# Kernel optimization log

Measured on AMD Instinct MI355X. Metric: run time of the kernel, lower is better.

## Reference

```python
import jax, jax.numpy as jnp
import numpy as np

DEGREE = 3
FEATURES = 512
N_BSPLINES = 64
BATCH = 2048
WINDOW = DEGREE + 2  # unfold window size: degree + 2
N_KNOTS = N_BSPLINES + DEGREE + 1


def setup_inputs() -> dict:
    key = jax.random.key(0)
    kx, kw = jax.random.split(key)
    x = jax.random.uniform(kx, (BATCH, FEATURES), dtype=jnp.float32)  # in [0,1] = interval
    # reset_parameter(): linspace over interval broadcast to all features
    knots = jnp.broadcast_to(
        jnp.linspace(0.0, 1.0, N_KNOTS, dtype=jnp.float32), (FEATURES, N_KNOTS)
    )
    # weights are zero-init in the module; use small random values for a meaningful baseline
    weights = jax.random.normal(kw, (FEATURES, N_BSPLINES), dtype=jnp.float32) * 0.1
    return {"x": x, "knots": knots, "weights": weights}


def reference(x, knots, weights):
    # knots.unfold(-1, degree+2, 1) -> (F, N, W) sliding windows
    idx = jnp.arange(N_BSPLINES)[:, None] + jnp.arange(WINDOW)[None, :]  # (N, W)
    kwin = knots[:, idx]  # (F, N, W)
    # relu^degree of (x - knot) differences: (B, F, N, W)
    relu = jnp.maximum(x[..., None, None] - kwin, 0.0) ** DEGREE
    # pairwise knot differences + eye: dif[i, j] = kwin[j] - kwin[i] + delta_ij
    knot_dif = kwin[..., None, :] - kwin[..., :, None] + jnp.eye(WINDOW, dtype=knots.dtype)  # (F, N, W, W)
    coef = 1.0 / jnp.prod(knot_dif, axis=-1)  # (F, N, W) divided-difference coefficients
    spline = jnp.sum(relu * coef, axis=-1)  # vecdot over window -> (B, F, N)
    return jnp.sum(spline * weights, axis=-1)  # vecdot over splines -> (B, F)
```

## Files before the change

### kernel.cpp

```cpp
#include <hip/hip_runtime.h>

#pragma clang fp contract(off)

#define FEATURES   512
#define N_BSPLINES 64
#define N_KNOTS    68
#define WINDOW     5
#define BATCH      2048

#define TF 16
#define TB 64
#define QPT 4
#define NT 256
#define TSTRIDE 516

__device__ __forceinline__ float cube_f32(float r) {
    float s = r * r;
    return s * r;
}

__global__ __launch_bounds__(NT) void bspline_fused(
    const float* __restrict__ x, const float* __restrict__ knots,
    const float* __restrict__ weights, float* __restrict__ out)
{
    __shared__ float kL[N_KNOTS * TF];
    __shared__ float tab[TF * TSTRIDE];

    const int tid  = threadIdx.x;
    const int fblk = blockIdx.x & (FEATURES / TF - 1);
    const int bblk = blockIdx.x >> 5;
    const int f0   = fblk * TF;
    const int b0   = bblk * TB;

    const int ft = tid & (TF - 1);
    const int bt = tid >> 4;

    float xq[QPT];
    #pragma unroll
    for (int q = 0; q < QPT; ++q)
        xq[q] = x[(b0 + bt + q * 16) * FEATURES + f0 + ft];

    for (int e = tid; e < N_KNOTS * TF; e += NT) {
        int ff = e & (TF - 1), t = e >> 4;
        kL[t * TF + ff] = knots[(f0 + ff) * N_KNOTS + t];
    }
    __syncthreads();

    for (int e = tid; e < N_BSPLINES * WINDOW * TF; e += NT) {
        int ff = e & (TF - 1);
        int m  = e >> 4;
        int i = m / WINDOW, j = m % WINDOW;
        float kj = kL[(i + j) * TF + ff];
        float prod = 1.0f;
        #pragma unroll
        for (int b = 0; b < WINDOW; ++b) {
            float df = (b == j) ? 1.0f : (kL[(i + b) * TF + ff] - kj);
            prod = prod * df;
        }
        tab[ff * TSTRIDE + i * 8 + j] = 1.0f / prod;
    }
    for (int e = tid; e < N_BSPLINES * TF; e += NT) {
        int ff = e & (TF - 1);
        int i  = e >> 4;
        tab[ff * TSTRIDE + i * 8 + 5] = weights[(f0 + ff) * N_BSPLINES + i];
        tab[ff * TSTRIDE + i * 8 + 6] =
            (i < N_BSPLINES - 1) ? kL[(i + 5) * TF + ff] : 0.0f;
    }
    __syncthreads();

    const float* __restrict__ row = &tab[ft * TSTRIDE];

    float acc[QPT], r0[QPT], r1[QPT], r2[QPT], r3[QPT], r4[QPT];
    #pragma unroll
    for (int q = 0; q < QPT; ++q) {
        acc[q] = 0.0f;
        r0[q] = cube_f32(fmaxf(xq[q] - kL[0 * TF + ft], 0.0f));
        r1[q] = cube_f32(fmaxf(xq[q] - kL[1 * TF + ft], 0.0f));
        r2[q] = cube_f32(fmaxf(xq[q] - kL[2 * TF + ft], 0.0f));
        r3[q] = cube_f32(fmaxf(xq[q] - kL[3 * TF + ft], 0.0f));
        r4[q] = cube_f32(fmaxf(xq[q] - kL[4 * TF + ft], 0.0f));
    }

    #pragma unroll 8
    for (int i = 0; i < N_BSPLINES; ++i) {
        const float4 cv = *(const float4*)&row[i * 8];
        const float4 cw = *(const float4*)&row[i * 8 + 4];
        #pragma unroll
        for (int q = 0; q < QPT; ++q) {
            float m0 = r0[q] * cv.x;
            float m1 = r1[q] * cv.y;
            float m2 = r2[q] * cv.z;
            float m3 = r3[q] * cv.w;
            float m4 = r4[q] * cw.x;
            float t04  = m0 + m4;
            float t042 = t04 + m2;
            float t13  = m1 + m3;
            float sp   = t042 + t13;
            acc[q] = acc[q] + sp * cw.y;
            r0[q] = r1[q]; r1[q] = r2[q]; r2[q] = r3[q]; r3[q] = r4[q];
            r4[q] = cube_f32(fmaxf(xq[q] - cw.z, 0.0f));
        }
    }

    #pragma unroll
    for (int q = 0; q < QPT; ++q)
        out[(b0 + bt + q * 16) * FEATURES + f0 + ft] = acc[q];
}

extern "C" void kernel_launch(void* const* d_in, const int* in_sizes, int n_in,
                              void* d_out, int out_size, void* d_ws, size_t ws_size,
                              hipStream_t stream) {
    const float* x       = (const float*)d_in[0];
    const float* knots   = (const float*)d_in[1];
    const float* weights = (const float*)d_in[2];
    float*       out     = (float*)d_out;

    const int blocks = (FEATURES / TF) * (BATCH / TB);
    bspline_fused<<<blocks, NT, 0, stream>>>(x, knots, weights, out);
}
```

Measured before the change: 89.91 us.

## Split coefficient table into prep kernel and double per-thread batch work

Moves the divided-difference coefficient, weight and knot table construction into a separate per-feature prep kernel that writes to workspace. The eval kernel then copies the ready table into shared memory with float4 loads instead of recomputing it in every batch block. Batch rows per block and per thread are doubled to amortize the table load. The register rotation is unrolled manually so the shifts between window registers disappear. This adds a second kernel launch and roughly doubles live registers per thread, which may lower occupancy.

```diff
diff --git a/kernel.cpp b/kernel.cpp
--- a/kernel.cpp
+++ b/kernel.cpp
@@ -9,8 +9,8 @@
 #define BATCH      2048
 
 #define TF 16
-#define TB 64
-#define QPT 4
+#define TB 128
+#define QPT 8
 #define NT 256
 #define TSTRIDE 516
 
@@ -19,11 +19,53 @@
     return s * r;
 }
 
-__global__ __launch_bounds__(NT) void bspline_fused(
+__global__ __launch_bounds__(320) void bspline_prep(
+    const float* __restrict__ knots, const float* __restrict__ weights,
+    float* __restrict__ g)
+{
+    const int f = blockIdx.x;
+    const int t = threadIdx.x;
+    const float* kf = knots + f * N_KNOTS;
+    const int i = t / WINDOW, j = t % WINDOW;
+    float kj = kf[i + j];
+    float prod = 1.0f;
+    #pragma unroll
+    for (int b = 0; b < WINDOW; ++b) {
+        float df = (b == j) ? 1.0f : (kf[i + b] - kj);
+        prod = prod * df;
+    }
+    g[f * TSTRIDE + i * 8 + j] = 1.0f / prod;
+    if (t < N_BSPLINES) {
+        g[f * TSTRIDE + t * 8 + 5] = weights[f * N_BSPLINES + t];
+        g[f * TSTRIDE + t * 8 + 6] = (t < N_BSPLINES - 1) ? kf[t + 5] : 0.0f;
+        g[f * TSTRIDE + t * 8 + 7] = 0.0f;
+    }
+}
+
+#define STEP(I, RA, RB, RC, RD, RE)                                         \
+    do {                                                                    \
+        const float4 cv = *(const float4*)&row[(I) * 8];        \
+        const float4 cw = *(const float4*)&row[(I) * 8 + 4];   \
+        _Pragma("unroll")                                                   \
+        for (int q = 0; q < QPT; ++q) {                                     \
+            float m0 = RA[q] * cv.x;                                        \
+            float m1 = RB[q] * cv.y;                                        \
+            float m2 = RC[q] * cv.z;                                        \
+            float m3 = RD[q] * cv.w;                                        \
+            float m4 = RE[q] * cw.x;                                        \
+            float t04  = m0 + m4;                 \
+            float t042 = t04 + m2;                                          \
+            float t13  = m1 + m3;                                           \
+            float sp   = t042 + t13;                                        \
+            acc[q] = acc[q] + sp * cw.y;      \
+            RA[q] = cube_f32(fmaxf(xq[q] - cw.z, 0.0f));                    \
+        }                                                                   \
+    } while (0)
+
+__global__ __launch_bounds__(NT) void bspline_eval(
     const float* __restrict__ x, const float* __restrict__ knots,
-    const float* __restrict__ weights, float* __restrict__ out)
+    const float* __restrict__ coefg, float* __restrict__ out)
 {
-    __shared__ float kL[N_KNOTS * TF];
     __shared__ float tab[TF * TSTRIDE];
 
     const int tid  = threadIdx.x;
@@ -31,41 +73,20 @@
     const int bblk = blockIdx.x >> 5;
     const int f0   = fblk * TF;
     const int b0   = bblk * TB;
-
-    const int ft = tid & (TF - 1);
-    const int bt = tid >> 4;
+    const int ft   = tid & (TF - 1);
+    const int bt   = tid >> 4;
 
     float xq[QPT];
     #pragma unroll
     for (int q = 0; q < QPT; ++q)
         xq[q] = x[(b0 + bt + q * 16) * FEATURES + f0 + ft];
+    const float* kf = knots + (f0 + ft) * N_KNOTS;
+    float k0 = kf[0], k1 = kf[1], k2 = kf[2], k3 = kf[3], k4 = kf[4];
 
-    for (int e = tid; e < N_KNOTS * TF; e += NT) {
-        int ff = e & (TF - 1), t = e >> 4;
-        kL[t * TF + ff] = knots[(f0 + ff) * N_KNOTS + t];
-    }
-    __syncthreads();
-
-    for (int e = tid; e < N_BSPLINES * WINDOW * TF; e += NT) {
-        int ff = e & (TF - 1);
-        int m  = e >> 4;
-        int i = m / WINDOW, j = m % WINDOW;
-        float kj = kL[(i + j) * TF + ff];
-        float prod = 1.0f;
-        #pragma unroll
-        for (int b = 0; b < WINDOW; ++b) {
-            float df = (b == j) ? 1.0f : (kL[(i + b) * TF + ff] - kj);
-            prod = prod * df;
-        }
-        tab[ff * TSTRIDE + i * 8 + j] = 1.0f / prod;
-    }
-    for (int e = tid; e < N_BSPLINES * TF; e += NT) {
-        int ff = e & (TF - 1);
-        int i  = e >> 4;
-        tab[ff * TSTRIDE + i * 8 + 5] = weights[(f0 + ff) * N_BSPLINES + i];
-        tab[ff * TSTRIDE + i * 8 + 6] =
-            (i < N_BSPLINES - 1) ? kL[(i + 5) * TF + ff] : 0.0f;
-    }
+    const float4* __restrict__ gsrc = (const float4*)(coefg + (size_t)f0 * TSTRIDE);
+    float4* __restrict__ tabv = (float4*)tab;
+    for (int e = tid; e < TF * TSTRIDE / 4; e += NT)
+        tabv[e] = gsrc[e];
     __syncthreads();
 
     const float* __restrict__ row = &tab[ft * TSTRIDE];
@@ -74,33 +95,25 @@
     #pragma unroll
     for (int q = 0; q < QPT; ++q) {
         acc[q] = 0.0f;
-        r0[q] = cube_f32(fmaxf(xq[q] - kL[0 * TF + ft], 0.0f));
-        r1[q] = cube_f32(fmaxf(xq[q] - kL[1 * TF + ft], 0.0f));
-        r2[q] = cube_f32(fmaxf(xq[q] - kL[2 * TF + ft], 0.0f));
-        r3[q] = cube_f32(fmaxf(xq[q] - kL[3 * TF + ft], 0.0f));
-        r4[q] = cube_f32(fmaxf(xq[q] - kL[4 * TF + ft], 0.0f));
+        r0[q] = cube_f32(fmaxf(xq[q] - k0, 0.0f));
+        r1[q] = cube_f32(fmaxf(xq[q] - k1, 0.0f));
+        r2[q] = cube_f32(fmaxf(xq[q] - k2, 0.0f));
+        r3[q] = cube_f32(fmaxf(xq[q] - k3, 0.0f));
+        r4[q] = cube_f32(fmaxf(xq[q] - k4, 0.0f));
     }
 
-    #pragma unroll 8
-    for (int i = 0; i < N_BSPLINES; ++i) {
-        const float4 cv = *(const float4*)&row[i * 8];
-        const float4 cw = *(const float4*)&row[i * 8 + 4];
-        #pragma unroll
-        for (int q = 0; q < QPT; ++q) {
-            float m0 = r0[q] * cv.x;
-            float m1 = r1[q] * cv.y;
-            float m2 = r2[q] * cv.z;
-            float m3 = r3[q] * cv.w;
-            float m4 = r4[q] * cw.x;
-            float t04  = m0 + m4;
-            float t042 = t04 + m2;
-            float t13  = m1 + m3;
-            float sp   = t042 + t13;
-            acc[q] = acc[q] + sp * cw.y;
-            r0[q] = r1[q]; r1[q] = r2[q]; r2[q] = r3[q]; r3[q] = r4[q];
-            r4[q] = cube_f32(fmaxf(xq[q] - cw.z, 0.0f));
-        }
+    for (int gi = 0; gi < 12; ++gi) {
+        const int i = gi * 5;
+        STEP(i + 0, r0, r1, r2, r3, r4);
+        STEP(i + 1, r1, r2, r3, r4, r0);
+        STEP(i + 2, r2, r3, r4, r0, r1);
+        STEP(i + 3, r3, r4, r0, r1, r2);
+        STEP(i + 4, r4, r0, r1, r2, r3);
     }
+    STEP(60, r0, r1, r2, r3, r4);
+    STEP(61, r1, r2, r3, r4, r0);
+    STEP(62, r2, r3, r4, r0, r1);
+    STEP(63, r3, r4, r0, r1, r2);
 
     #pragma unroll
     for (int q = 0; q < QPT; ++q)
@@ -114,7 +127,10 @@
     const float* knots   = (const float*)d_in[1];
     const float* weights = (const float*)d_in[2];
     float*       out     = (float*)d_out;
+    float*       coefg   = (float*)d_ws;
+
+    bspline_prep<<<FEATURES, 320, 0, stream>>>(knots, weights, coefg);
 
     const int blocks = (FEATURES / TF) * (BATCH / TB);
-    bspline_fused<<<blocks, NT, 0, stream>>>(x, knots, weights, out);
+    bspline_eval<<<blocks, NT, 0, stream>>>(x, knots, coefg, out);
 }
```

Result: faster. 86.43 us (-3.9%).
